# Optimization experiments

Measured on AMD Instinct MI355X. Metric: run time of the kernel, lower is better.

Reference implementation:

```python
import jax, jax.numpy as jnp
import numpy as np

N_NODES = 50000
N_EDGES = 400000
IN_DIM = 128
HID_DIM = 128
OUT_DIM = 128


def setup_inputs() -> dict:
    key = jax.random.key(0)
    k_x, k_e, k_w1, k_b1, k_w2, k_b2 = jax.random.split(key, 6)
    x = jax.random.normal(k_x, (N_NODES, IN_DIM), dtype=jnp.float32)
    edge_index = jax.random.randint(k_e, (2, N_EDGES), 0, N_NODES, dtype=jnp.int64)
    # nn.Linear-style params: W is [out, in], kaiming-uniform-ish init
    lim1 = 1.0 / np.sqrt(IN_DIM)
    lim2 = 1.0 / np.sqrt(HID_DIM)
    W1 = jax.random.uniform(k_w1, (HID_DIM, IN_DIM), jnp.float32, -lim1, lim1)
    b1 = jax.random.uniform(k_b1, (HID_DIM,), jnp.float32, -lim1, lim1)
    W2 = jax.random.uniform(k_w2, (OUT_DIM, HID_DIM), jnp.float32, -lim2, lim2)
    b2 = jax.random.uniform(k_b2, (OUT_DIM,), jnp.float32, -lim2, lim2)
    return {"x": x, "edge_index": edge_index, "W1": W1, "b1": b1, "W2": W2, "b2": b2}


def reference(x, edge_index, W1, b1, W2, b2):
    # h = relu(fc1(x));  dropout in eval mode -> identity
    h = jax.nn.relu(x @ W1.T + b1)                      # [N, hid]
    src, dst = edge_index[0], edge_index[1]
    # gather messages from src, scatter-add (mean) into dst
    agg = jax.ops.segment_sum(h[src], dst, num_segments=N_NODES)      # [N, hid]
    deg = jax.ops.segment_sum(jnp.ones_like(dst, dtype=h.dtype), dst,
                              num_segments=N_NODES)                   # [N]
    deg = jnp.maximum(deg, 1.0)
    agg = agg / deg[:, None]
    # residual add + fc2
    return (agg + h) @ W2.T + b2                        # [N, out]
```

## Files before the change

kernel.cpp:

```cpp
#include <hip/hip_runtime.h>

#define N_NODES 50000
#define N_EDGES 400000
#define DIM 128
#define BUCKET_BLK ((N_EDGES + 255) / 256)
#define FC1_BLK ((N_NODES + 63) / 64)

typedef unsigned short u16;
typedef unsigned int   u32;
typedef __bf16 v8bf  __attribute__((ext_vector_type(8)));
typedef float  f32x4 __attribute__((ext_vector_type(4)));
typedef u16    u16x8 __attribute__((ext_vector_type(8)));

union BF8 { u16x8 u; v8bf b; };

__device__ __forceinline__ float bf2f(u16 u) {
    union { u32 i; float f; } v; v.i = ((u32)u) << 16; return v.f;
}
__device__ __forceinline__ u16 f2bf(float f) {
    union { float f; u32 i; } v; v.f = f; u32 u = v.i;
    return (u16)((u + 0x7FFFu + ((u >> 16) & 1u)) >> 16);
}

__global__ __launch_bounds__(256, 3) void build_fc1_kernel(
    const int* __restrict__ esrc, const int* __restrict__ edst,
    int* __restrict__ head, int2* __restrict__ pairbuf,
    const float* __restrict__ x, const float* __restrict__ W1,
    const float* __restrict__ b1, u16* __restrict__ h)
{
    __shared__ u16 xs[64 * 136];
    const int bid = blockIdx.x;

    if (bid < BUCKET_BLK) {
        int e = bid * 256 + threadIdx.x;
        if (e < N_EDGES) {
            int src = esrc[e], dst = edst[e];
            if ((unsigned)src < N_NODES && (unsigned)dst < N_NODES) {
                int old = atomicExch(&head[dst], e);
                pairbuf[e] = make_int2(old, src);
            }
        }
        return;
    }

    const int t = threadIdx.x;
    const int wave = t >> 6, lane = t & 63, quad = lane >> 4, l15 = lane & 15;
    const int ch = wave >> 1, rh = wave & 1;
    const int row0 = (bid - BUCKET_BLK) * 64;

    BF8 barr[4][4];
#pragma unroll
    for (int ct = 0; ct < 4; ++ct)
#pragma unroll
        for (int ks = 0; ks < 4; ++ks) {
            const float* wp = W1 + (size_t)(ch * 64 + ct * 16 + l15) * DIM
                                 + ks * 32 + quad * 8;
            float4 f0 = *(const float4*)wp;
            float4 f1 = *(const float4*)(wp + 4);
            u16x8 p;
            p[0] = f2bf(f0.x); p[1] = f2bf(f0.y); p[2] = f2bf(f0.z); p[3] = f2bf(f0.w);
            p[4] = f2bf(f1.x); p[5] = f2bf(f1.y); p[6] = f2bf(f1.z); p[7] = f2bf(f1.w);
            barr[ct][ks].u = p;
        }

    {
        int srow = t >> 2, k0 = (t & 3) * 32;
        int grow = row0 + srow; if (grow >= N_NODES) grow = N_NODES - 1;
        const float* xp = x + (size_t)grow * DIM + k0;
#pragma unroll
        for (int j = 0; j < 4; ++j) {
            float4 f0 = *(const float4*)(xp + j * 8);
            float4 f1 = *(const float4*)(xp + j * 8 + 4);
            u16x8 p;
            p[0] = f2bf(f0.x); p[1] = f2bf(f0.y); p[2] = f2bf(f0.z); p[3] = f2bf(f0.w);
            p[4] = f2bf(f1.x); p[5] = f2bf(f1.y); p[6] = f2bf(f1.z); p[7] = f2bf(f1.w);
            *(u16x8*)&xs[srow * 136 + k0 + j * 8] = p;
        }
    }

    f32x4 acc[2][4];
#pragma unroll
    for (int ct = 0; ct < 4; ++ct) {
        float bv = b1[ch * 64 + ct * 16 + l15];
        acc[0][ct] = (f32x4){bv, bv, bv, bv};
        acc[1][ct] = (f32x4){bv, bv, bv, bv};
    }
    __syncthreads();

#pragma unroll
    for (int ks = 0; ks < 4; ++ks) {
        BF8 a0, a1;
        a0.u = *(const u16x8*)&xs[(rh * 32 +  0 + l15) * 136 + ks * 32 + quad * 8];
        a1.u = *(const u16x8*)&xs[(rh * 32 + 16 + l15) * 136 + ks * 32 + quad * 8];
#pragma unroll
        for (int ct = 0; ct < 4; ++ct) {
            acc[0][ct] = __builtin_amdgcn_mfma_f32_16x16x32_bf16(
                a0.b, barr[ct][ks].b, acc[0][ct], 0, 0, 0);
            acc[1][ct] = __builtin_amdgcn_mfma_f32_16x16x32_bf16(
                a1.b, barr[ct][ks].b, acc[1][ct], 0, 0, 0);
        }
    }

#pragma unroll
    for (int rt = 0; rt < 2; ++rt)
#pragma unroll
        for (int i = 0; i < 4; ++i) {
            int row = row0 + rh * 32 + rt * 16 + quad * 4 + i;
            if (row < N_NODES) {
#pragma unroll
                for (int ct = 0; ct < 4; ++ct) {
                    int col = ch * 64 + ct * 16 + l15;
                    h[(size_t)row * DIM + col] = f2bf(fmaxf(acc[rt][ct][i], 0.f));
                }
            }
        }
}

__global__ __launch_bounds__(256) void aggregate_kernel(
    const int* __restrict__ head, const int2* __restrict__ pairbuf,
    const u16* __restrict__ h, u16* __restrict__ z)
{
    const int wave = threadIdx.x >> 6;
    const int lane = threadIdx.x & 63;
    const int n = blockIdx.x * 4 + wave;
    if (n >= N_NODES) return;

    float a0 = 0.f, a1 = 0.f;
    int deg = 0;
    int e = head[n];
    if (e >= 0) {
        int2 p = pairbuf[e];
        while (true) {
            const int en  = p.x;
            const int src = p.y;
            u32 v = *(const u32*)(h + (size_t)src * DIM + lane * 2);
            int2 pn;
            const bool more = (en >= 0);
            if (more) pn = pairbuf[en];
            a0 += bf2f((u16)v); a1 += bf2f((u16)(v >> 16));
            ++deg;
            if (!more) break;
            p = pn;
        }
    }

    float inv = (deg > 0) ? 1.f / (float)deg : 1.f;
    u32 r = *(const u32*)(h + (size_t)n * DIM + lane * 2);
    float z0 = a0 * inv + bf2f((u16)r);
    float z1 = a1 * inv + bf2f((u16)(r >> 16));
    u32 pck = (u32)f2bf(z0) | ((u32)f2bf(z1) << 16);
    *(u32*)(z + (size_t)n * DIM + lane * 2) = pck;
}

__global__ __launch_bounds__(256, 3) void fc2_mfma(
    const u16* __restrict__ z, const float* __restrict__ W2,
    const float* __restrict__ b2, float* __restrict__ out)
{
    __shared__ u16 xs[64 * 136];
    const int t = threadIdx.x;
    const int wave = t >> 6, lane = t & 63, quad = lane >> 4, l15 = lane & 15;
    const int ch = wave >> 1, rh = wave & 1;
    const int row0 = blockIdx.x * 64;

    BF8 barr[4][4];
#pragma unroll
    for (int ct = 0; ct < 4; ++ct)
#pragma unroll
        for (int ks = 0; ks < 4; ++ks) {
            const float* wp = W2 + (size_t)(ch * 64 + ct * 16 + l15) * DIM
                                 + ks * 32 + quad * 8;
            float4 f0 = *(const float4*)wp;
            float4 f1 = *(const float4*)(wp + 4);
            u16x8 p;
            p[0] = f2bf(f0.x); p[1] = f2bf(f0.y); p[2] = f2bf(f0.z); p[3] = f2bf(f0.w);
            p[4] = f2bf(f1.x); p[5] = f2bf(f1.y); p[6] = f2bf(f1.z); p[7] = f2bf(f1.w);
            barr[ct][ks].u = p;
        }

    {
        int srow = t >> 1, k0 = (t & 1) * 64;
        int grow = row0 + srow; if (grow >= N_NODES) grow = N_NODES - 1;
        const u16* zp = z + (size_t)grow * DIM + k0;
#pragma unroll
        for (int j = 0; j < 8; ++j)
            *(u16x8*)&xs[srow * 136 + k0 + j * 8] = *(const u16x8*)(zp + j * 8);
    }

    f32x4 acc[2][4];
#pragma unroll
    for (int ct = 0; ct < 4; ++ct) {
        float bv = b2[ch * 64 + ct * 16 + l15];
        acc[0][ct] = (f32x4){bv, bv, bv, bv};
        acc[1][ct] = (f32x4){bv, bv, bv, bv};
    }
    __syncthreads();

#pragma unroll
    for (int ks = 0; ks < 4; ++ks) {
        BF8 a0, a1;
        a0.u = *(const u16x8*)&xs[(rh * 32 +  0 + l15) * 136 + ks * 32 + quad * 8];
        a1.u = *(const u16x8*)&xs[(rh * 32 + 16 + l15) * 136 + ks * 32 + quad * 8];
#pragma unroll
        for (int ct = 0; ct < 4; ++ct) {
            acc[0][ct] = __builtin_amdgcn_mfma_f32_16x16x32_bf16(
                a0.b, barr[ct][ks].b, acc[0][ct], 0, 0, 0);
            acc[1][ct] = __builtin_amdgcn_mfma_f32_16x16x32_bf16(
                a1.b, barr[ct][ks].b, acc[1][ct], 0, 0, 0);
        }
    }

#pragma unroll
    for (int rt = 0; rt < 2; ++rt)
#pragma unroll
        for (int i = 0; i < 4; ++i) {
            int row = row0 + rh * 32 + rt * 16 + quad * 4 + i;
            if (row < N_NODES) {
#pragma unroll
                for (int ct = 0; ct < 4; ++ct) {
                    int col = ch * 64 + ct * 16 + l15;
                    out[(size_t)row * DIM + col] = acc[rt][ct][i];
                }
            }
        }
}

extern "C" void kernel_launch(void* const* d_in, const int* in_sizes, int n_in,
                              void* d_out, int out_size, void* d_ws, size_t ws_size,
                              hipStream_t stream)
{
    const float* x  = (const float*)d_in[0];
    const int*   ei = (const int*)d_in[1];
    const float* W1 = (const float*)d_in[2];
    const float* b1 = (const float*)d_in[3];
    const float* W2 = (const float*)d_in[4];
    const float* b2 = (const float*)d_in[5];
    float* out = (float*)d_out;

    const int* esrc = ei;
    const int* edst = ei + N_EDGES;

    char* ws = (char*)d_ws;
    size_t off = 0;
    u16*  h       = (u16*)(ws + off);  off += (size_t)N_NODES * DIM * 2;
    u16*  z       = (u16*)(ws + off);  off += (size_t)N_NODES * DIM * 2;
    int*  head    = (int*)(ws + off);  off += (size_t)N_NODES * 4;
    int2* pairbuf = (int2*)(ws + off); off += (size_t)N_EDGES * 8;

    hipMemsetAsync(head, 0xFF, (size_t)N_NODES * 4, stream);

    build_fc1_kernel<<<BUCKET_BLK + FC1_BLK, 256, 0, stream>>>(
        esrc, edst, head, pairbuf, x, W1, b1, h);
    aggregate_kernel<<<(N_NODES + 3) / 4, 256, 0, stream>>>(
        head, pairbuf, h, z);
    fc2_mfma<<<(N_NODES + 63) / 64, 256, 0, stream>>>(z, W2, b2, out);
}
```

Before: 179.3 us.

## Fuse neighbor aggregation into fc2 kernel, staging z tile in shared memory

Merges the aggregation kernel into the fc2 MFMA kernel. Each block now walks the edge linked lists for its 64 rows and writes the bf16 z rows straight into the shared-memory tile, so the z intermediate no longer goes to global memory and one launch is removed. The work mapping also changes: 16 lanes per node, each loading 8 bf16 values, so a wave handles 4 nodes at once instead of 1 node per wave with 2 values per lane. The linked-list walks are serialized within each wave and prefetching of the next pair entry is dropped, so latency hiding and divergence across nodes of different degree may get worse.

```diff
diff --git a/kernel.cpp b/kernel.cpp
--- a/kernel.cpp
+++ b/kernel.cpp
@@ -116,51 +116,45 @@
         }
 }
 
-__global__ __launch_bounds__(256) void aggregate_kernel(
+__global__ __launch_bounds__(256, 3) void agg_fc2_kernel(
     const int* __restrict__ head, const int2* __restrict__ pairbuf,
-    const u16* __restrict__ h, u16* __restrict__ z)
-{
-    const int wave = threadIdx.x >> 6;
-    const int lane = threadIdx.x & 63;
-    const int n = blockIdx.x * 4 + wave;
-    if (n >= N_NODES) return;
-
-    float a0 = 0.f, a1 = 0.f;
-    int deg = 0;
-    int e = head[n];
-    if (e >= 0) {
-        int2 p = pairbuf[e];
-        while (true) {
-            const int en  = p.x;
-            const int src = p.y;
-            u32 v = *(const u32*)(h + (size_t)src * DIM + lane * 2);
-            int2 pn;
-            const bool more = (en >= 0);
-            if (more) pn = pairbuf[en];
-            a0 += bf2f((u16)v); a1 += bf2f((u16)(v >> 16));
-            ++deg;
-            if (!more) break;
-            p = pn;
-        }
-    }
-
-    float inv = (deg > 0) ? 1.f / (float)deg : 1.f;
-    u32 r = *(const u32*)(h + (size_t)n * DIM + lane * 2);
-    float z0 = a0 * inv + bf2f((u16)r);
-    float z1 = a1 * inv + bf2f((u16)(r >> 16));
-    u32 pck = (u32)f2bf(z0) | ((u32)f2bf(z1) << 16);
-    *(u32*)(z + (size_t)n * DIM + lane * 2) = pck;
-}
-
-__global__ __launch_bounds__(256, 3) void fc2_mfma(
-    const u16* __restrict__ z, const float* __restrict__ W2,
+    const u16* __restrict__ h, const float* __restrict__ W2,
     const float* __restrict__ b2, float* __restrict__ out)
 {
     __shared__ u16 xs[64 * 136];
     const int t = threadIdx.x;
-    const int wave = t >> 6, lane = t & 63, quad = lane >> 4, l15 = lane & 15;
-    const int ch = wave >> 1, rh = wave & 1;
+    const int wv = t >> 6, lane = t & 63, quad = lane >> 4, l15 = lane & 15;
     const int row0 = blockIdx.x * 64;
+
+#pragma unroll 1
+    for (int r = 0; r < 4; ++r) {
+        const int s = wv * 16 + r * 4 + quad;
+        const int n = row0 + s;
+        float a[8];
+#pragma unroll
+        for (int j = 0; j < 8; ++j) a[j] = 0.f;
+        int deg = 0;
+        u16x8 pk = (u16x8){0, 0, 0, 0, 0, 0, 0, 0};
+        if (n < N_NODES) {
+            int e = head[n];
+            while (e >= 0) {
+                int2 p = pairbuf[e];
+                u16x8 v = *(const u16x8*)(h + (size_t)p.y * DIM + l15 * 8);
+                e = p.x;
+                ++deg;
+#pragma unroll
+                for (int j = 0; j < 8; ++j) a[j] += bf2f(v[j]);
+            }
+            u16x8 hres = *(const u16x8*)(h + (size_t)n * DIM + l15 * 8);
+            float inv = (deg > 0) ? 1.f / (float)deg : 1.f;
+#pragma unroll
+            for (int j = 0; j < 8; ++j)
+                pk[j] = f2bf(a[j] * inv + bf2f(hres[j]));
+        }
+        *(u16x8*)&xs[s * 136 + l15 * 8] = pk;
+    }
+
+    const int ch = wv >> 1, rh = wv & 1;
 
     BF8 barr[4][4];
 #pragma unroll
@@ -176,15 +170,6 @@
             p[4] = f2bf(f1.x); p[5] = f2bf(f1.y); p[6] = f2bf(f1.z); p[7] = f2bf(f1.w);
             barr[ct][ks].u = p;
         }
-
-    {
-        int srow = t >> 1, k0 = (t & 1) * 64;
-        int grow = row0 + srow; if (grow >= N_NODES) grow = N_NODES - 1;
-        const u16* zp = z + (size_t)grow * DIM + k0;
-#pragma unroll
-        for (int j = 0; j < 8; ++j)
-            *(u16x8*)&xs[srow * 136 + k0 + j * 8] = *(const u16x8*)(zp + j * 8);
-    }
 
     f32x4 acc[2][4];
 #pragma unroll
@@ -242,7 +227,6 @@
     char* ws = (char*)d_ws;
     size_t off = 0;
     u16*  h       = (u16*)(ws + off);  off += (size_t)N_NODES * DIM * 2;
-    u16*  z       = (u16*)(ws + off);  off += (size_t)N_NODES * DIM * 2;
     int*  head    = (int*)(ws + off);  off += (size_t)N_NODES * 4;
     int2* pairbuf = (int2*)(ws + off); off += (size_t)N_EDGES * 8;
 
@@ -250,7 +234,6 @@
 
     build_fc1_kernel<<<BUCKET_BLK + FC1_BLK, 256, 0, stream>>>(
         esrc, edst, head, pairbuf, x, W1, b1, h);
-    aggregate_kernel<<<(N_NODES + 3) / 4, 256, 0, stream>>>(
-        head, pairbuf, h, z);
-    fc2_mfma<<<(N_NODES + 63) / 64, 256, 0, stream>>>(z, W2, b2, out);
-}
+    agg_fc2_kernel<<<FC1_BLK, 256, 0, stream>>>(
+        head, pairbuf, h, W2, b2, out);
+}
```

After: 197.6 us. 10.2% more time.
